# Kernel optimization log

Hardware: AMD Instinct MI355X
Metric: run time of the kernel (lower is better)

Reference implementation:

```python
import jax, jax.numpy as jnp
import numpy as np

LOG2PI = float(np.log(2.0 * np.pi))
B, S, K, D = 64, 512, 64, 16


def setup_inputs() -> dict:
    key = jax.random.key(0)
    k1, k2, k3, k4 = jax.random.split(key, 4)
    z = jax.random.randint(k1, (B, S), 0, K)                       # categorical input
    z_noise = jax.random.normal(k2, (B * S, 1, D), dtype=jnp.float32)  # prior sample z_cont
    t = 0.1 * jax.random.normal(k3, (K, D), dtype=jnp.float32)     # ExtActFixed per-category shift
    log_s = 0.1 * jax.random.normal(k4, (K, D), dtype=jnp.float32) # ExtActFixed per-category log-scale
    return {"z": z, "z_noise": z_noise, "t": t, "log_s": log_s}


def _std_normal_logp(x):
    return -0.5 * x * x - 0.5 * LOG2PI


def reference(z, z_noise, t, log_s):
    b, s = z.shape
    n_cat, d = t.shape
    categ = z.reshape(-1)                                  # [N]
    zc = z_noise                                           # [N,1,D]

    init_log_p = jnp.sum(_std_normal_logp(zc), axis=(1, 2))  # [N]

    # conditional affine flow, forward direction
    t_c = t[categ][:, None, :]                             # gather [N,1,D]
    s_c = log_s[categ][:, None, :]
    z_enc = (zc + t_c) * jnp.exp(s_c)                      # [N,1,D]
    ldj_fwd = jnp.sum(s_c, axis=(1, 2))                    # [N]

    cat_prior = -jnp.log(jnp.float32(n_cat))               # log_softmax(zeros)
    log_point = init_log_p - ldj_fwd + cat_prior           # [N]

    # expand-to-K: inverse flow for every category (broadcast, no explicit tile)
    z_back = z_enc * jnp.exp(-log_s)[None] - t[None]       # [N,K,D]
    back_log_p = jnp.sum(_std_normal_logp(z_back), axis=-1)  # [N,K]
    ldj_back = -jnp.sum(log_s, axis=-1)[None]              # [1,K]
    denom = back_log_p + ldj_back + cat_prior              # [N,K]

    # swap in exact point prob for the true category
    mask = jax.nn.one_hot(categ, n_cat, dtype=denom.dtype) # [N,K]
    denom = denom * (1.0 - mask) + log_point[:, None] * mask
    log_den = jax.nn.logsumexp(denom, axis=-1)             # [N]
    class_prob_log = log_point - log_den                   # [N]

    # beta=1, channel_padding_mask=ones
    ldj_loc = class_prob_log - (init_log_p - ldj_fwd)      # [N]

    z_out = z_enc.reshape(b, s, d)
    ldj = ldj_loc.reshape(b, s).sum(axis=-1)               # [B]
    return z_out, ldj
```

## Files before the change

### kernel.cpp

```cpp
#include <hip/hip_runtime.h>
#include <math.h>

#define NTOT   32768
#define BATCH  64
#define KCAT   64
#define DDIM   16
#define F_LOG2PI 1.8378770664093453f
#define CAT_PRIOR -4.1588830833596715f

constexpr int LPN  = 8;
constexpr int GPN  = 2;
constexpr int BLK  = 256;
constexpr int NPB  = (BLK / LPN) * GPN;
constexpr int NBLK = NTOT / NPB;
constexpr int ROWS = 36;

__global__ __launch_bounds__(BLK, 2) void lce_main(
    const int*   __restrict__ z,
    const float* __restrict__ zn,
    const float* __restrict__ t,
    const float* __restrict__ ls,
    float*       __restrict__ out,
    float*       __restrict__ partial)
{
    __shared__ float comb[KCAT * ROWS];
    __shared__ float est [KCAT * ROWS];
    __shared__ float red[4];

    const int tid = threadIdx.x;

    for (int i = tid; i < KCAT * DDIM; i += BLK) {
        const int k = i >> 4, d = i & 15;
        const float lv = ls[i];
        comb[k * ROWS + d]      = expf(-lv);
        comb[k * ROWS + 16 + d] = t[i];
        est [k * ROWS + d]      = expf(lv);
    }
    if (tid < KCAT) {
        float s = 0.f;
        #pragma unroll
        for (int d = 0; d < DDIM; ++d) s += ls[tid * DDIM + d];
        comb[tid * ROWS + 32] = -0.5f * F_LOG2PI * DDIM - s + CAT_PRIOR;
        comb[tid * ROWS + 33] = s;
    }
    __syncthreads();

    const int q  = tid & (LPN - 1);
    const int n0 = blockIdx.x * NPB + (tid >> 3) * GPN;

    float ze[GPN][DDIM];
    float log_point[GPN], base[GPN];
    int   cat[GPN];

    #pragma unroll
    for (int nn = 0; nn < GPN; ++nn) {
        const int n = n0 + nn;
        const int c = z[n];
        cat[nn] = c;
        const float sumls = comb[c * ROWS + 33];
        const float4* zp = (const float4*)(zn + (long)n * DDIM);
        float ss = 0.f;
        #pragma unroll
        for (int j = 0; j < 4; ++j) {
            const float4 v  = zp[j];
            const float4 tc = *(const float4*)&comb[c * ROWS + 16 + j * 4];
            const float4 ec = *(const float4*)&est [c * ROWS + j * 4];
            ze[nn][j*4+0] = (v.x + tc.x) * ec.x;
            ze[nn][j*4+1] = (v.y + tc.y) * ec.y;
            ze[nn][j*4+2] = (v.z + tc.z) * ec.z;
            ze[nn][j*4+3] = (v.w + tc.w) * ec.w;
            ss = fmaf(v.x, v.x, ss);
            ss = fmaf(v.y, v.y, ss);
            ss = fmaf(v.z, v.z, ss);
            ss = fmaf(v.w, v.w, ss);
        }
        const float init_lp = -0.5f * ss - 8.f * F_LOG2PI;
        base[nn]      = init_lp - sumls;
        log_point[nn] = base[nn] + CAT_PRIOR;
    }

    float dn[GPN][KCAT / LPN];
    float mx[GPN];
    #pragma unroll
    for (int nn = 0; nn < GPN; ++nn) mx[nn] = -1e30f;

    #pragma unroll
    for (int j = 0; j < KCAT / LPN; ++j) {
        const int k = q + j * LPN;
        float is_[DDIM], tr[DDIM];
        #pragma unroll
        for (int jj = 0; jj < 4; ++jj) {
            *(float4*)&is_[jj*4] = *(const float4*)&comb[k * ROWS + jj * 4];
            *(float4*)&tr [jj*4] = *(const float4*)&comb[k * ROWS + 16 + jj * 4];
        }
        const float kc = comb[k * ROWS + 32];
        #pragma unroll
        for (int nn = 0; nn < GPN; ++nn) {
            float acc = 0.f;
            #pragma unroll
            for (int d = 0; d < DDIM; ++d) {
                const float zb = fmaf(ze[nn][d], is_[d], -tr[d]);
                acc = fmaf(zb, zb, acc);
            }
            float dv = fmaf(-0.5f, acc, kc);
            dn[nn][j] = (k == cat[nn]) ? log_point[nn] : dv;
            mx[nn] = fmaxf(mx[nn], dn[nn][j]);
        }
    }

    float ldj_acc = 0.f;
    #pragma unroll
    for (int nn = 0; nn < GPN; ++nn) {
        float m = mx[nn];
        m = fmaxf(m, __shfl_xor(m, 1));
        m = fmaxf(m, __shfl_xor(m, 2));
        m = fmaxf(m, __shfl_xor(m, 4));
        float se = 0.f;
        #pragma unroll
        for (int j = 0; j < KCAT / LPN; ++j) se += __expf(dn[nn][j] - m);
        se += __shfl_xor(se, 1);
        se += __shfl_xor(se, 2);
        se += __shfl_xor(se, 4);
        const float log_den = m + __logf(se);
        ldj_acc += (log_point[nn] - log_den) - base[nn];
    }

    float4* op = (float4*)(out + (long)n0 * DDIM);
#define CH(nn, jj) make_float4(ze[nn][4*(jj)+0], ze[nn][4*(jj)+1], ze[nn][4*(jj)+2], ze[nn][4*(jj)+3])
    switch (q) {
        case 0: op[0] = CH(0,0); break;
        case 1: op[1] = CH(0,1); break;
        case 2: op[2] = CH(0,2); break;
        case 3: op[3] = CH(0,3); break;
        case 4: op[4] = CH(1,0); break;
        case 5: op[5] = CH(1,1); break;
        case 6: op[6] = CH(1,2); break;
        case 7: op[7] = CH(1,3); break;
    }
#undef CH

    float v = ldj_acc;
    v += __shfl_xor(v, 8);
    v += __shfl_xor(v, 16);
    v += __shfl_xor(v, 32);
    if ((tid & 63) == 0) red[tid >> 6] = v;
    __syncthreads();
    if (tid == 0) partial[blockIdx.x] = red[0] + red[1] + red[2] + red[3];
}

__global__ void lce_fin(const float* __restrict__ partial, float* __restrict__ ldj)
{
    const int b = threadIdx.x;
    if (b < BATCH) {
        const float4* p4 = (const float4*)(partial + b * 8);
        const float4 a = p4[0], c = p4[1];
        ldj[b] = ((a.x + a.y) + (a.z + a.w)) + ((c.x + c.y) + (c.z + c.w));
    }
}

extern "C" void kernel_launch(void* const* d_in, const int* in_sizes, int n_in,
                              void* d_out, int out_size, void* d_ws, size_t ws_size,
                              hipStream_t stream)
{
    const int*   z  = (const int*)  d_in[0];
    const float* zn = (const float*)d_in[1];
    const float* t  = (const float*)d_in[2];
    const float* ls = (const float*)d_in[3];
    float* out     = (float*)d_out;
    float* ldj     = out + (long)NTOT * DDIM;
    float* partial = (float*)d_ws;

    lce_main<<<NBLK, BLK, 0, stream>>>(z, zn, t, ls, out, partial);
    lce_fin<<<1, 64, 0, stream>>>(partial, ldj);
}
```

Before: 13.01 us.

## Fuse final per-batch reduction into main kernel via last-block atomic counter

Removes the separate finalize kernel: each block stores its partial sum, bumps a per-batch atomic counter, and the eighth block to arrive sums the eight partials and writes ldj. This drops the second kernel's dispatch but adds a memset launch to zero the counters each call, plus atomic traffic. Ordering relies on relaxed atomics and an explicit vmcnt wait rather than a release/acquire fence.

```diff
diff --git a/kernel.cpp b/kernel.cpp
--- a/kernel.cpp
+++ b/kernel.cpp
@@ -21,7 +21,9 @@
     const float* __restrict__ t,
     const float* __restrict__ ls,
     float*       __restrict__ out,
-    float*       __restrict__ partial)
+    float*       __restrict__ ldj,
+    float*       __restrict__ partial,
+    unsigned*    __restrict__ cnt)
 {
     __shared__ float comb[KCAT * ROWS];
     __shared__ float est [KCAT * ROWS];
@@ -145,16 +147,24 @@
     v += __shfl_xor(v, 32);
     if ((tid & 63) == 0) red[tid >> 6] = v;
     __syncthreads();
-    if (tid == 0) partial[blockIdx.x] = red[0] + red[1] + red[2] + red[3];
-}
 
-__global__ void lce_fin(const float* __restrict__ partial, float* __restrict__ ldj)
-{
-    const int b = threadIdx.x;
-    if (b < BATCH) {
-        const float4* p4 = (const float4*)(partial + b * 8);
-        const float4 a = p4[0], c = p4[1];
-        ldj[b] = ((a.x + a.y) + (a.z + a.w)) + ((c.x + c.y) + (c.z + c.w));
+    if (tid == 0) {
+        const float own = red[0] + red[1] + red[2] + red[3];
+        const int bb = blockIdx.x >> 3;
+        __hip_atomic_store(&partial[blockIdx.x], own,
+                           __ATOMIC_RELAXED, __HIP_MEMORY_SCOPE_AGENT);
+        asm volatile("s_waitcnt vmcnt(0)" ::: "memory");
+        const unsigned old = __hip_atomic_fetch_add(&cnt[bb], 1u,
+                           __ATOMIC_RELAXED, __HIP_MEMORY_SCOPE_AGENT);
+        if (old == 7u) {
+            float p[8];
+            #pragma unroll
+            for (int j = 0; j < 8; ++j)
+                p[j] = __hip_atomic_load(&partial[bb * 8 + j],
+                           __ATOMIC_RELAXED, __HIP_MEMORY_SCOPE_AGENT);
+            ldj[bb] = ((p[0] + p[1]) + (p[2] + p[3]))
+                    + ((p[4] + p[5]) + (p[6] + p[7]));
+        }
     }
 }
 
@@ -169,7 +179,8 @@
     float* out     = (float*)d_out;
     float* ldj     = out + (long)NTOT * DDIM;
     float* partial = (float*)d_ws;
+    unsigned* cnt  = (unsigned*)((char*)d_ws + NBLK * sizeof(float));
 
-    lce_main<<<NBLK, BLK, 0, stream>>>(z, zn, t, ls, out, partial);
-    lce_fin<<<1, 64, 0, stream>>>(partial, ldj);
+    hipMemsetAsync(cnt, 0, BATCH * sizeof(unsigned), stream);
+    lce_main<<<NBLK, BLK, 0, stream>>>(z, zn, t, ls, out, ldj, partial, cnt);
 }
```

After: 18.54 us. 42.5% more time.
